# Performance work log

Hardware: AMD Instinct MI355X
Metric: run time of the kernel (lower is better)

The kernel has to match this reference:

```python
import jax, jax.numpy as jnp
import numpy as np

B, S_IN, S_CTX = 2, 4096, 512
INPUT_DIM = CTX_DIM = DIM = 1024
NUM_HEADS = 16
HEAD_DIM = DIM // NUM_HEADS
BASE = 10000.0


def rms_norm(x, scale, eps=1e-6):
    xf = x.astype(jnp.float32)
    rrms = jax.lax.rsqrt(jnp.mean(xf * xf, axis=-1, keepdims=True) + eps)
    return (xf * rrms).astype(x.dtype) * scale


def apply_rope(x, pos):
    # x: [B, N, H, D]; rotate-half RoPE over full head_dim
    d = x.shape[-1]
    inv_freq = 1.0 / (BASE ** (jnp.arange(0, d, 2, dtype=jnp.float32) / d))  # [d/2]
    ang = pos.astype(jnp.float32)[:, None] * inv_freq[None, :]  # [N, d/2]
    cos = jnp.cos(ang)[None, :, None, :]
    sin = jnp.sin(ang)[None, :, None, :]
    x1, x2 = x[..., : d // 2], x[..., d // 2 :]
    return jnp.concatenate([x1 * cos - x2 * sin, x2 * cos + x1 * sin], axis=-1).astype(x.dtype)


def setup_inputs() -> dict:
    key = jax.random.key(0)
    ks = jax.random.split(key, 8)
    std = 0.02
    return {
        "input": jax.random.normal(ks[0], (B, S_IN, INPUT_DIM), jnp.float32),
        "context": jax.random.normal(ks[1], (B, S_CTX, CTX_DIM), jnp.float32),
        "W_qkv_in": jax.random.normal(ks[2], (3 * DIM, INPUT_DIM), jnp.float32) * std,
        "b_qkv_in": jnp.zeros((3 * DIM,), jnp.float32),
        "W_qkv_ctx": jax.random.normal(ks[3], (3 * DIM, CTX_DIM), jnp.float32) * std,
        "b_qkv_ctx": jnp.zeros((3 * DIM,), jnp.float32),
        "q_scale_in": jnp.ones((DIM,), jnp.float32),
        "k_scale_in": jnp.ones((DIM,), jnp.float32),
        "q_scale_ctx": jnp.ones((DIM,), jnp.float32),
        "k_scale_ctx": jnp.ones((DIM,), jnp.float32),
        "W_out_in": jax.random.normal(ks[4], (INPUT_DIM, DIM), jnp.float32) * std,
        "b_out_in": jnp.zeros((INPUT_DIM,), jnp.float32),
        "W_out_ctx": jax.random.normal(ks[5], (CTX_DIM, DIM), jnp.float32) * std,
        "b_out_ctx": jnp.zeros((CTX_DIM,), jnp.float32),
    }


def reference(input, context, W_qkv_in, b_qkv_in, W_qkv_ctx, b_qkv_ctx,
              q_scale_in, k_scale_in, q_scale_ctx, k_scale_ctx,
              W_out_in, b_out_in, W_out_ctx, b_out_ctx):
    # dual-stream QKV projections
    qkv_i = input @ W_qkv_in.T + b_qkv_in        # [B, S_in, 3*DIM]
    qkv_c = context @ W_qkv_ctx.T + b_qkv_ctx    # [B, S_ctx, 3*DIM]
    qi, ki, vi = jnp.split(qkv_i, 3, axis=-1)
    qc, kc, vc = jnp.split(qkv_c, 3, axis=-1)
    # QK-RMSNorm over full dim (as in QKNorm(dim))
    qi, ki = rms_norm(qi, q_scale_in), rms_norm(ki, k_scale_in)
    qc, kc = rms_norm(qc, q_scale_ctx), rms_norm(kc, k_scale_ctx)
    # concat context first, then input
    q = jnp.concatenate([qc, qi], axis=1)  # [B, N, DIM]
    k = jnp.concatenate([kc, ki], axis=1)
    v = jnp.concatenate([vc, vi], axis=1)
    N = q.shape[1]
    pos = jnp.arange(N)
    # RoPE applied per head
    q = apply_rope(q.reshape(B, N, NUM_HEADS, HEAD_DIM), pos).reshape(B, N, DIM)
    k = apply_rope(k.reshape(B, N, NUM_HEADS, HEAD_DIM), pos).reshape(B, N, DIM)
    # single-head attention over full dim (faithful to source: heads flattened before q@k^T)
    scale = HEAD_DIM ** -0.5
    attn = jax.nn.softmax(jnp.einsum('bnd,bmd->bnm', q, k) * scale, axis=-1)
    out = jnp.einsum('bnm,bmd->bnd', attn, v)  # [B, N, DIM]
    s_ctx = context.shape[1]
    input_output = out[:, s_ctx:, :] @ W_out_in.T + b_out_in
    context_output = out[:, :s_ctx, :] @ W_out_ctx.T + b_out_ctx
    return (input_output, context_output)
```

## Files before the change

kernel.cpp:

```cpp
#include <hip/hip_runtime.h>
#include <stdint.h>

typedef unsigned short u16;
typedef __bf16 bf16x8 __attribute__((ext_vector_type(8)));
typedef float f32x4 __attribute__((ext_vector_type(4)));

typedef const __attribute__((address_space(1))) uint32_t* gu32p;
typedef __attribute__((address_space(3))) uint32_t* lu32p;
#define GLOAD_LDS16(g, l) \
  __builtin_amdgcn_global_load_lds((gu32p)(const void*)(g), (lu32p)(void*)(l), 16, 0, 0)

static __device__ __forceinline__ u16 f2bf(float f) {
  uint32_t u = __builtin_bit_cast(uint32_t, f);
  return (u16)((u + 0x7FFFu + ((u >> 16) & 1u)) >> 16);
}
static __device__ __forceinline__ float bf2f(u16 h) {
  uint32_t u = ((uint32_t)h) << 16;
  return __builtin_bit_cast(float, u);
}

__global__ __launch_bounds__(256) void k_conv_all(
    const float* __restrict__ s0, u16* __restrict__ d0,
    const float* __restrict__ s1, u16* __restrict__ d1,
    const float* __restrict__ s2, u16* __restrict__ d2,
    const float* __restrict__ s3, u16* __restrict__ d3,
    const float* __restrict__ s4, u16* __restrict__ d4,
    const float* __restrict__ s5, u16* __restrict__ d5) {
  int b = blockIdx.x;
  const float* src; u16* dst; long off;
  if (b < 8192)       { src = s0; dst = d0; off = (long)b * 1024; }
  else if (b < 9216)  { src = s1; dst = d1; off = (long)(b - 8192) * 1024; }
  else if (b < 12288) { src = s2; dst = d2; off = (long)(b - 9216) * 1024; }
  else if (b < 15360) { src = s3; dst = d3; off = (long)(b - 12288) * 1024; }
  else if (b < 16384) { src = s4; dst = d4; off = (long)(b - 15360) * 1024; }
  else                { src = s5; dst = d5; off = (long)(b - 16384) * 1024; }
  long i = off + threadIdx.x * 4;
  const float4 v = *(const float4*)&src[i];
  ushort4 o;
  o.x = f2bf(v.x); o.y = f2bf(v.y); o.z = f2bf(v.z); o.w = f2bf(v.w);
  *(ushort4*)&dst[i] = o;
}

__device__ __forceinline__ void gemm_m97(const u16* __restrict__ A, const u16* __restrict__ Bt,
                                         int lda, int ldb, long row0, long col0,
                                         int kbeg, int kend, u16* smem, f32x4 acc[4][4]) {
  const int tid = threadIdx.x;
  const int l = tid & 63;
  const int w = tid >> 6;
  const int wm = w >> 1, wn = w & 1;
  const int lr = l & 15, kg = l >> 4;
  const int rs = (kg ^ ((lr >> 1) & 3)) * 8;
  const int r_l = tid >> 2;
  const int ssrc = ((tid & 3) ^ ((r_l >> 1) & 3)) * 8;
  const u16* gA = &A[(row0 + r_l) * (long)lda + ssrc];
  const u16* gB = &Bt[(col0 + r_l) * (long)ldb + ssrc];
  const int wofs = w * 512;

  for (int k0 = kbeg; k0 < kend; k0 += 32) {
    GLOAD_LDS16(gA + k0, smem + wofs);
    GLOAD_LDS16(gA + 64 * (long)lda + k0, smem + 2048 + wofs);
    GLOAD_LDS16(gB + k0, smem + 4096 + wofs);
    GLOAD_LDS16(gB + 64 * (long)ldb + k0, smem + 6144 + wofs);
    __syncthreads();
    bf16x8 af[4], bv[4];
#pragma unroll
    for (int i = 0; i < 4; ++i) {
      af[i] = *(const bf16x8*)&smem[(wm * 64 + i * 16 + lr) * 32 + rs];
      bv[i] = *(const bf16x8*)&smem[4096 + (wn * 64 + i * 16 + lr) * 32 + rs];
    }
#pragma unroll
    for (int mf = 0; mf < 4; ++mf)
#pragma unroll
      for (int nf = 0; nf < 4; ++nf)
        acc[mf][nf] = __builtin_amdgcn_mfma_f32_16x16x32_bf16(af[mf], bv[nf], acc[mf][nf], 0, 0, 0);
    __syncthreads();
  }
}

#define EPI_VARS                                   \
  const int l = threadIdx.x & 63;                  \
  const int w = threadIdx.x >> 6;                  \
  const int wm = w >> 1, wn = w & 1;               \
  const int mrow = (l >> 4) * 4, ncol = l & 15;

__global__ __launch_bounds__(256) void k_gemm_qkv(
    const u16* __restrict__ XIN, const u16* __restrict__ XCTX,
    const u16* __restrict__ WQI, const u16* __restrict__ WQC,
    const float* __restrict__ bqi, const float* __restrict__ bqc,
    u16* __restrict__ qb, u16* __restrict__ kb, u16* __restrict__ vt) {
  __shared__ u16 smem[8192];
  f32x4 acc[4][4] = {};
  const bool isCtx = blockIdx.x >= 64;
  const u16* X = isCtx ? XCTX : XIN;
  const u16* W = isCtx ? WQC : WQI;
  const float* bias = isCtx ? bqc : bqi;
  const int seg_start = isCtx ? 0 : 512;
  long row0 = (long)(isCtx ? blockIdx.x - 64 : blockIdx.x) * 128;
  long col0 = (long)blockIdx.y * 128;
  gemm_m97(X, W, 1024, 1024, row0, col0, 0, 1024, smem, acc);
  EPI_VARS
#pragma unroll
  for (int mf = 0; mf < 4; ++mf)
#pragma unroll
    for (int nf = 0; nf < 4; ++nf)
#pragma unroll
      for (int r = 0; r < 4; ++r) {
        int m = (int)row0 + wm * 64 + mf * 16 + mrow + r;
        int n = (int)col0 + wn * 64 + nf * 16 + ncol;
        float v = acc[mf][nf][r] + bias[n];
        int b, s;
        if (isCtx) { b = m >> 9; s = m & 511; } else { b = m >> 12; s = m & 4095; }
        long grow = (long)b * 4608 + seg_start + s;
        if (n < 1024)      qb[grow * 1024 + n] = f2bf(v);
        else if (n < 2048) kb[grow * 1024 + (n - 1024)] = f2bf(v);
        else               vt[((long)b * 1024 + (n - 2048)) * 4608 + seg_start + s] = f2bf(v);
      }
}

__global__ __launch_bounds__(256) void k_normrope(u16* __restrict__ qb, u16* __restrict__ kb,
                                                  const float* __restrict__ qsi, const float* __restrict__ ksi,
                                                  const float* __restrict__ qsc, const float* __restrict__ ksc) {
  __shared__ float sm[4];
  const int row = blockIdx.x;
  const int which = blockIdx.y;
  const int n = row % 4608;
  u16* buf = which ? kb : qb;
  const float* scale = which ? (n < 512 ? ksc : ksi) : (n < 512 ? qsc : qsi);
  u16* rp = buf + (long)row * 1024;
  const int t = threadIdx.x;
  const int h = t >> 4;
  const int jj = (t & 15) * 2;
  const int e1 = h * 64 + jj;
  const int e2 = e1 + 32;
  uint32_t u1 = *(const uint32_t*)&rp[e1];
  uint32_t u2 = *(const uint32_t*)&rp[e2];
  float x1a = bf2f((u16)u1), x1b = bf2f((u16)(u1 >> 16));
  float x2a = bf2f((u16)u2), x2b = bf2f((u16)(u2 >> 16));
  float ss = x1a * x1a + x1b * x1b + x2a * x2a + x2b * x2b;
#pragma unroll
  for (int o = 32; o; o >>= 1) ss += __shfl_xor(ss, o, 64);
  if ((t & 63) == 0) sm[t >> 6] = ss;
  __syncthreads();
  ss = sm[0] + sm[1] + sm[2] + sm[3];
  const float rr = rsqrtf(ss * (1.0f / 1024.0f) + 1e-6f);
  float s1a = scale[e1], s1b = scale[e1 + 1], s2a = scale[e2], s2b = scale[e2 + 1];
  x1a *= rr * s1a; x1b *= rr * s1b; x2a *= rr * s2a; x2b *= rr * s2b;
  const float c = -13.287712379549449f / 32.0f;
  float fa = exp2f((float)jj * c), fb = exp2f((float)(jj + 1) * c);
  float sna, csa, snb, csb;
  sincosf((float)n * fa, &sna, &csa);
  sincosf((float)n * fb, &snb, &csb);
  u16 o1a = f2bf(x1a * csa - x2a * sna), o1b = f2bf(x1b * csb - x2b * snb);
  u16 o2a = f2bf(x2a * csa + x1a * sna), o2b = f2bf(x2b * csb + x1b * snb);
  *(uint32_t*)&rp[e1] = (uint32_t)o1a | ((uint32_t)o1b << 16);
  *(uint32_t*)&rp[e2] = (uint32_t)o2a | ((uint32_t)o2b << 16);
}

__global__ __launch_bounds__(256) void k_gemm_s(const u16* __restrict__ Q, const u16* __restrict__ Kb,
                                                float* __restrict__ S) {
  __shared__ u16 smem[8192];
  f32x4 acc[4][4] = {};
  long row0 = (long)blockIdx.x * 128;
  long col0 = (long)blockIdx.y * 128;
  gemm_m97(Q, Kb, 1024, 1024, row0, col0, 0, 1024, smem, acc);
  EPI_VARS
#pragma unroll
  for (int mf = 0; mf < 4; ++mf)
#pragma unroll
    for (int nf = 0; nf < 4; ++nf)
#pragma unroll
      for (int r = 0; r < 4; ++r) {
        long m = row0 + wm * 64 + mf * 16 + mrow + r;
        long n = col0 + wn * 64 + nf * 16 + ncol;
        S[m * 4608 + n] = acc[mf][nf][r] * 0.125f;
      }
}

__global__ __launch_bounds__(256) void k_softmax(const float* __restrict__ S, u16* __restrict__ P) {
  __shared__ float sm[4];
  const long row = blockIdx.x;
  const float* sr = S + row * 4608;
  const int t = threadIdx.x;
  float v[18];
  float mx = -3.4e38f;
#pragma unroll
  for (int i = 0; i < 18; ++i) { v[i] = sr[i * 256 + t]; mx = fmaxf(mx, v[i]); }
#pragma unroll
  for (int o = 32; o; o >>= 1) mx = fmaxf(mx, __shfl_xor(mx, o, 64));
  if ((t & 63) == 0) sm[t >> 6] = mx;
  __syncthreads();
  mx = fmaxf(fmaxf(sm[0], sm[1]), fmaxf(sm[2], sm[3]));
  __syncthreads();
  float sum = 0.f;
#pragma unroll
  for (int i = 0; i < 18; ++i) { v[i] = __expf(v[i] - mx); sum += v[i]; }
#pragma unroll
  for (int o = 32; o; o >>= 1) sum += __shfl_xor(sum, o, 64);
  if ((t & 63) == 0) sm[t >> 6] = sum;
  __syncthreads();
  sum = sm[0] + sm[1] + sm[2] + sm[3];
  const float inv = 1.0f / sum;
  u16* pr = P + row * 4608;
#pragma unroll
  for (int i = 0; i < 18; ++i) pr[i * 256 + t] = f2bf(v[i] * inv);
}

__global__ __launch_bounds__(256) void k_gemm_o(const u16* __restrict__ P, const u16* __restrict__ VT,
                                                float* __restrict__ OP) {
  __shared__ u16 smem[8192];
  f32x4 acc[4][4] = {};
  long row0 = (long)blockIdx.x * 128;
  long col0 = (long)blockIdx.y * 128;
  const int kc = blockIdx.z;
  gemm_m97(P, VT, 4608, 4608, row0, col0, kc * 2304, (kc + 1) * 2304, smem, acc);
  float* op = OP + (long)kc * 4608 * 1024;
  EPI_VARS
#pragma unroll
  for (int mf = 0; mf < 4; ++mf)
#pragma unroll
    for (int nf = 0; nf < 4; ++nf)
#pragma unroll
      for (int r = 0; r < 4; ++r) {
        long m = row0 + wm * 64 + mf * 16 + mrow + r;
        long n = col0 + wn * 64 + nf * 16 + ncol;
        op[m * 1024 + n] = acc[mf][nf][r];
      }
}

__global__ __launch_bounds__(256) void k_reduce2(const float* __restrict__ OP, u16* __restrict__ AO) {
  const long st = 4608L * 1024;
  long i = ((long)blockIdx.x * 256 + threadIdx.x) * 4;
  float4 a = *(const float4*)&OP[i];
  float4 b = *(const float4*)&OP[i + st];
  ushort4 o;
  o.x = f2bf(a.x + b.x);
  o.y = f2bf(a.y + b.y);
  o.z = f2bf(a.z + b.z);
  o.w = f2bf(a.w + b.w);
  *(ushort4*)&AO[i] = o;
}

__global__ __launch_bounds__(256) void k_gemm_out2(const u16* __restrict__ AO,
                                                   const u16* __restrict__ WOI, const u16* __restrict__ WOC,
                                                   const float* __restrict__ boi, const float* __restrict__ boc,
                                                   float* __restrict__ out) {
  __shared__ u16 smem[8192];
  f32x4 acc[4][4] = {};
  long row0 = (long)blockIdx.x * 128;
  long col0 = (long)blockIdx.y * 128;
  int b = (int)(row0 / 4608);
  int s0 = (int)(row0 % 4608);
  const bool ctx = s0 < 512;
  const u16* W = ctx ? WOC : WOI;
  const float* bias = ctx ? boc : boi;
  float* ob = ctx ? out + 8388608 + ((long)b * 512 + s0) * 1024
                  : out + ((long)b * 4096 + (s0 - 512)) * 1024;
  gemm_m97(AO, W, 1024, 1024, row0, col0, 0, 1024, smem, acc);
  EPI_VARS
#pragma unroll
  for (int mf = 0; mf < 4; ++mf)
#pragma unroll
    for (int nf = 0; nf < 4; ++nf)
#pragma unroll
      for (int r = 0; r < 4; ++r) {
        long m = wm * 64 + mf * 16 + mrow + r;
        long n = col0 + wn * 64 + nf * 16 + ncol;
        ob[m * 1024 + n] = acc[mf][nf][r] + bias[n];
      }
}

extern "C" void kernel_launch(void* const* d_in, const int* in_sizes, int n_in,
                              void* d_out, int out_size, void* d_ws, size_t ws_size,
                              hipStream_t stream) {
  const float* input   = (const float*)d_in[0];
  const float* context = (const float*)d_in[1];
  const float* Wqi     = (const float*)d_in[2];
  const float* bqi     = (const float*)d_in[3];
  const float* Wqc     = (const float*)d_in[4];
  const float* bqc     = (const float*)d_in[5];
  const float* qsi     = (const float*)d_in[6];
  const float* ksi     = (const float*)d_in[7];
  const float* qsc     = (const float*)d_in[8];
  const float* ksc     = (const float*)d_in[9];
  const float* Woi     = (const float*)d_in[10];
  const float* boi     = (const float*)d_in[11];
  const float* Woc     = (const float*)d_in[12];
  const float* boc     = (const float*)d_in[13];
  float* out = (float*)d_out;

  uint8_t* ws = (uint8_t*)d_ws;
  u16* XIN  = (u16*)(ws + 0);
  u16* XCTX = (u16*)(ws + 16777216);
  u16* WQI  = (u16*)(ws + 18874368);
  u16* WQC  = (u16*)(ws + 25165824);
  u16* WOI  = (u16*)(ws + 31457280);
  u16* WOC  = (u16*)(ws + 33554432);
  u16* QB   = (u16*)(ws + 35651584);
  u16* KB   = (u16*)(ws + 54525952);
  u16* VT   = (u16*)(ws + 73400320);
  u16* AO   = (u16*)(ws + 92274688);
  float* S32 = (float*)(ws + 111149056);
  u16* PB   = (u16*)(ws + 196083712);

  k_conv_all<<<dim3(17408), 256, 0, stream>>>(input, XIN, context, XCTX, Wqi, WQI,
                                              Wqc, WQC, Woi, WOI, Woc, WOC);

  k_gemm_qkv<<<dim3(72, 24), 256, 0, stream>>>(XIN, XCTX, WQI, WQC, bqi, bqc, QB, KB, VT);

  k_normrope<<<dim3(9216, 2), 256, 0, stream>>>(QB, KB, qsi, ksi, qsc, ksc);

  for (int b = 0; b < 2; ++b) {
    const u16* Qb  = QB + (long)b * 4608 * 1024;
    const u16* Kbp = KB + (long)b * 4608 * 1024;
    const u16* VTb = VT + (long)b * 1024 * 4608;
    u16* AOb = AO + (long)b * 4608 * 1024;
    k_gemm_s<<<dim3(36, 36), 256, 0, stream>>>(Qb, Kbp, S32);
    k_softmax<<<dim3(4608), 256, 0, stream>>>(S32, PB);
    k_gemm_o<<<dim3(36, 8, 2), 256, 0, stream>>>(PB, VTb, (float*)S32);
    k_reduce2<<<dim3(4608), 256, 0, stream>>>((const float*)S32, AOb);
  }

  k_gemm_out2<<<dim3(72, 8), 256, 0, stream>>>(AO, WOI, WOC, boi, boc, out);
}
```

Before: 524.3 us.

## Replace GEMM core with 256x256 double-buffered pipelined 8-wave tile

Swaps the 128x128 single-buffered GEMM core for a 256x256 tile run by 512 threads. The new core uses 64-wide K steps, double-buffered LDS, staged global-to-LDS prefetch interleaved with MFMA quads, and s_setprio to raise priority around the MFMA bursts. All four GEMM kernels move to it, and the PV GEMM's split-K goes from 2 to 4 with a matching 4-way reduce. The aim is more operand reuse per LDS load and overlap of loads with compute. The trade-off is fewer blocks (some grids fall below the CU count), 128KB of LDS per block, and more partial-sum traffic.

```diff
diff --git a/kernel.cpp b/kernel.cpp
--- a/kernel.cpp
+++ b/kernel.cpp
@@ -9,6 +9,7 @@
 typedef __attribute__((address_space(3))) uint32_t* lu32p;
 #define GLOAD_LDS16(g, l) \
   __builtin_amdgcn_global_load_lds((gu32p)(const void*)(g), (lu32p)(void*)(l), 16, 0, 0)
+#define MFMA16 __builtin_amdgcn_mfma_f32_16x16x32_bf16
 
 static __device__ __forceinline__ u16 f2bf(float f) {
   uint32_t u = __builtin_bit_cast(uint32_t, f);
@@ -41,71 +42,113 @@
   *(ushort4*)&dst[i] = o;
 }
 
-__device__ __forceinline__ void gemm_m97(const u16* __restrict__ A, const u16* __restrict__ Bt,
-                                         int lda, int ldb, long row0, long col0,
-                                         int kbeg, int kend, u16* smem, f32x4 acc[4][4]) {
+__device__ __forceinline__ void gemm8p(const u16* __restrict__ A, const u16* __restrict__ Bt,
+                                       int lda, int ldb, long row0, long col0,
+                                       int kbeg, int kend, u16* smem, f32x4 acc[8][4]) {
   const int tid = threadIdx.x;
   const int l = tid & 63;
-  const int w = tid >> 6;
-  const int wm = w >> 1, wn = w & 1;
+  const int wid = tid >> 6;
+  const int wm = wid >> 2, wn = wid & 3;
   const int lr = l & 15, kg = l >> 4;
-  const int rs = (kg ^ ((lr >> 1) & 3)) * 8;
-  const int r_l = tid >> 2;
-  const int ssrc = ((tid & 3) ^ ((r_l >> 1) & 3)) * 8;
-  const u16* gA = &A[(row0 + r_l) * (long)lda + ssrc];
-  const u16* gB = &Bt[(col0 + r_l) * (long)ldb + ssrc];
-  const int wofs = w * 512;
-
-  for (int k0 = kbeg; k0 < kend; k0 += 32) {
-    GLOAD_LDS16(gA + k0, smem + wofs);
-    GLOAD_LDS16(gA + 64 * (long)lda + k0, smem + 2048 + wofs);
-    GLOAD_LDS16(gB + k0, smem + 4096 + wofs);
-    GLOAD_LDS16(gB + 64 * (long)ldb + k0, smem + 6144 + wofs);
-    __syncthreads();
-    bf16x8 af[4], bv[4];
-#pragma unroll
-    for (int i = 0; i < 4; ++i) {
-      af[i] = *(const bf16x8*)&smem[(wm * 64 + i * 16 + lr) * 32 + rs];
-      bv[i] = *(const bf16x8*)&smem[4096 + (wn * 64 + i * 16 + lr) * 32 + rs];
-    }
-#pragma unroll
-    for (int mf = 0; mf < 4; ++mf)
-#pragma unroll
-      for (int nf = 0; nf < 4; ++nf)
-        acc[mf][nf] = __builtin_amdgcn_mfma_f32_16x16x32_bf16(af[mf], bv[nf], acc[mf][nf], 0, 0, 0);
-    __syncthreads();
+  const int rx = lr & 7;
+  const int r_l = tid >> 3;
+  const int ss8 = ((tid & 7) ^ (r_l & 7)) * 8;
+  const u16* gA = &A[(row0 + r_l) * (long)lda + kbeg + ss8];
+  const u16* gB = &Bt[(col0 + r_l) * (long)ldb + kbeg + ss8];
+  const int wofs = wid * 512;
+  const int NK = (kend - kbeg) >> 6;
+
+#define STG_B0(s) if ((s) < NK) { const long kk = (long)(s) * 64; \
+    u16* bb = smem + ((s) & 1) * 32768 + 16384 + wofs; \
+    GLOAD_LDS16(gB + kk, bb); GLOAD_LDS16(gB + 64 * (long)ldb + kk, bb + 4096); }
+#define STG_B1(s) if ((s) < NK) { const long kk = (long)(s) * 64; \
+    u16* bb = smem + ((s) & 1) * 32768 + 16384 + 8192 + wofs; \
+    GLOAD_LDS16(gB + 128 * (long)ldb + kk, bb); GLOAD_LDS16(gB + 192 * (long)ldb + kk, bb + 4096); }
+#define STG_AL(s) if ((s) < NK) { const long kk = (long)(s) * 64; \
+    u16* bb = smem + ((s) & 1) * 32768 + wofs; \
+    GLOAD_LDS16(gA + kk, bb); GLOAD_LDS16(gA + 128 * (long)lda + kk, bb + 8192); }
+#define STG_AH(s) if ((s) < NK) { const long kk = (long)(s) * 64; \
+    u16* bb = smem + ((s) & 1) * 32768 + 4096 + wofs; \
+    GLOAD_LDS16(gA + 64 * (long)lda + kk, bb); GLOAD_LDS16(gA + 192 * (long)lda + kk, bb + 8192); }
+
+#define LDA_(db, mf, ks) (*(const bf16x8*)&smem[(db) + (wm * 128 + (mf) * 16 + lr) * 64 + (((ks) * 4 + kg) ^ rx) * 8])
+#define LDB_(db, nf, ks) (*(const bf16x8*)&smem[(db) + 16384 + (wn * 64 + (nf) * 16 + lr) * 64 + (((ks) * 4 + kg) ^ rx) * 8])
+
+#define BAR_MID() do { __builtin_amdgcn_s_barrier(); \
+    asm volatile("s_waitcnt lgkmcnt(0)" ::: "memory"); \
+    __builtin_amdgcn_sched_barrier(0); } while (0)
+#define QUAD(mf0) do { \
+    __builtin_amdgcn_s_setprio(1); \
+    _Pragma("unroll") \
+    for (int nf = 0; nf < 4; ++nf) { \
+      acc[(mf0)][nf]     = MFMA16(a00, bv0[nf], acc[(mf0)][nf], 0, 0, 0); \
+      acc[(mf0) + 1][nf] = MFMA16(a10, bv0[nf], acc[(mf0) + 1][nf], 0, 0, 0); \
+      acc[(mf0)][nf]     = MFMA16(a01, bv1[nf], acc[(mf0)][nf], 0, 0, 0); \
+      acc[(mf0) + 1][nf] = MFMA16(a11, bv1[nf], acc[(mf0) + 1][nf], 0, 0, 0); } \
+    __builtin_amdgcn_s_setprio(0); \
+    __builtin_amdgcn_s_barrier(); } while (0)
+
+  STG_B0(0); STG_B1(0); STG_AL(0); STG_AH(0);
+  STG_B0(1); STG_B1(1); STG_AL(1);
+  asm volatile("s_waitcnt vmcnt(6)" ::: "memory");
+  __builtin_amdgcn_s_barrier();
+  __builtin_amdgcn_sched_barrier(0);
+
+  for (int k = 0; k < NK; ++k) {
+    const int db = (k & 1) * 32768;
+    bf16x8 bv0[4], bv1[4], a00, a01, a10, a11;
+#pragma unroll
+    for (int nf = 0; nf < 4; ++nf) { bv0[nf] = LDB_(db, nf, 0); bv1[nf] = LDB_(db, nf, 1); }
+    a00 = LDA_(db, 0, 0); a01 = LDA_(db, 0, 1); a10 = LDA_(db, 1, 0); a11 = LDA_(db, 1, 1);
+    STG_AH(k + 1);
+    BAR_MID(); QUAD(0);
+    a00 = LDA_(db, 2, 0); a01 = LDA_(db, 2, 1); a10 = LDA_(db, 3, 0); a11 = LDA_(db, 3, 1);
+    STG_B0(k + 2);
+    BAR_MID(); QUAD(2);
+    a00 = LDA_(db, 4, 0); a01 = LDA_(db, 4, 1); a10 = LDA_(db, 5, 0); a11 = LDA_(db, 5, 1);
+    STG_B1(k + 2);
+    BAR_MID(); QUAD(4);
+    a00 = LDA_(db, 6, 0); a01 = LDA_(db, 6, 1); a10 = LDA_(db, 7, 0); a11 = LDA_(db, 7, 1);
+    STG_AL(k + 2);
+    if (k + 2 < NK) asm volatile("s_waitcnt vmcnt(6)" ::: "memory");
+    else            asm volatile("s_waitcnt vmcnt(0)" ::: "memory");
+    BAR_MID(); QUAD(6);
   }
-}
-
-#define EPI_VARS                                   \
+#undef STG_B0
+#undef STG_B1
+#undef STG_AL
+#undef STG_AH
+}
+
+#define EPI8                                       \
   const int l = threadIdx.x & 63;                  \
-  const int w = threadIdx.x >> 6;                  \
-  const int wm = w >> 1, wn = w & 1;               \
+  const int wid = threadIdx.x >> 6;                \
+  const int wm = wid >> 2, wn = wid & 3;           \
   const int mrow = (l >> 4) * 4, ncol = l & 15;
 
-__global__ __launch_bounds__(256) void k_gemm_qkv(
+__global__ __launch_bounds__(512, 2) void k_gemm_qkv(
     const u16* __restrict__ XIN, const u16* __restrict__ XCTX,
     const u16* __restrict__ WQI, const u16* __restrict__ WQC,
     const float* __restrict__ bqi, const float* __restrict__ bqc,
     u16* __restrict__ qb, u16* __restrict__ kb, u16* __restrict__ vt) {
-  __shared__ u16 smem[8192];
-  f32x4 acc[4][4] = {};
-  const bool isCtx = blockIdx.x >= 64;
+  __shared__ u16 smem[65536];
+  f32x4 acc[8][4] = {};
+  const bool isCtx = blockIdx.x >= 32;
   const u16* X = isCtx ? XCTX : XIN;
   const u16* W = isCtx ? WQC : WQI;
   const float* bias = isCtx ? bqc : bqi;
   const int seg_start = isCtx ? 0 : 512;
-  long row0 = (long)(isCtx ? blockIdx.x - 64 : blockIdx.x) * 128;
-  long col0 = (long)blockIdx.y * 128;
-  gemm_m97(X, W, 1024, 1024, row0, col0, 0, 1024, smem, acc);
-  EPI_VARS
-#pragma unroll
-  for (int mf = 0; mf < 4; ++mf)
+  long row0 = (long)(isCtx ? blockIdx.x - 32 : blockIdx.x) * 256;
+  long col0 = (long)blockIdx.y * 256;
+  gemm8p(X, W, 1024, 1024, row0, col0, 0, 1024, smem, acc);
+  EPI8
+#pragma unroll
+  for (int mf = 0; mf < 8; ++mf)
 #pragma unroll
     for (int nf = 0; nf < 4; ++nf)
 #pragma unroll
       for (int r = 0; r < 4; ++r) {
-        int m = (int)row0 + wm * 64 + mf * 16 + mrow + r;
+        int m = (int)row0 + wm * 128 + mf * 16 + mrow + r;
         int n = (int)col0 + wn * 64 + nf * 16 + ncol;
         float v = acc[mf][nf][r] + bias[n];
         int b, s;
@@ -156,21 +199,21 @@
   *(uint32_t*)&rp[e2] = (uint32_t)o2a | ((uint32_t)o2b << 16);
 }
 
-__global__ __launch_bounds__(256) void k_gemm_s(const u16* __restrict__ Q, const u16* __restrict__ Kb,
-                                                float* __restrict__ S) {
-  __shared__ u16 smem[8192];
-  f32x4 acc[4][4] = {};
-  long row0 = (long)blockIdx.x * 128;
-  long col0 = (long)blockIdx.y * 128;
-  gemm_m97(Q, Kb, 1024, 1024, row0, col0, 0, 1024, smem, acc);
-  EPI_VARS
-#pragma unroll
-  for (int mf = 0; mf < 4; ++mf)
+__global__ __launch_bounds__(512, 2) void k_gemm_s(const u16* __restrict__ Q, const u16* __restrict__ Kb,
+                                                   float* __restrict__ S) {
+  __shared__ u16 smem[65536];
+  f32x4 acc[8][4] = {};
+  long row0 = (long)blockIdx.x * 256;
+  long col0 = (long)blockIdx.y * 256;
+  gemm8p(Q, Kb, 1024, 1024, row0, col0, 0, 1024, smem, acc);
+  EPI8
+#pragma unroll
+  for (int mf = 0; mf < 8; ++mf)
 #pragma unroll
     for (int nf = 0; nf < 4; ++nf)
 #pragma unroll
       for (int r = 0; r < 4; ++r) {
-        long m = row0 + wm * 64 + mf * 16 + mrow + r;
+        long m = row0 + wm * 128 + mf * 16 + mrow + r;
         long n = col0 + wn * 64 + nf * 16 + ncol;
         S[m * 4608 + n] = acc[mf][nf][r] * 0.125f;
       }
@@ -205,49 +248,51 @@
   for (int i = 0; i < 18; ++i) pr[i * 256 + t] = f2bf(v[i] * inv);
 }
 
-__global__ __launch_bounds__(256) void k_gemm_o(const u16* __restrict__ P, const u16* __restrict__ VT,
-                                                float* __restrict__ OP) {
-  __shared__ u16 smem[8192];
-  f32x4 acc[4][4] = {};
-  long row0 = (long)blockIdx.x * 128;
-  long col0 = (long)blockIdx.y * 128;
+__global__ __launch_bounds__(512, 2) void k_gemm_o(const u16* __restrict__ P, const u16* __restrict__ VT,
+                                                   float* __restrict__ OP) {
+  __shared__ u16 smem[65536];
+  f32x4 acc[8][4] = {};
+  long row0 = (long)blockIdx.x * 256;
+  long col0 = (long)blockIdx.y * 256;
   const int kc = blockIdx.z;
-  gemm_m97(P, VT, 4608, 4608, row0, col0, kc * 2304, (kc + 1) * 2304, smem, acc);
+  gemm8p(P, VT, 4608, 4608, row0, col0, kc * 1152, (kc + 1) * 1152, smem, acc);
   float* op = OP + (long)kc * 4608 * 1024;
-  EPI_VARS
-#pragma unroll
-  for (int mf = 0; mf < 4; ++mf)
+  EPI8
+#pragma unroll
+  for (int mf = 0; mf < 8; ++mf)
 #pragma unroll
     for (int nf = 0; nf < 4; ++nf)
 #pragma unroll
       for (int r = 0; r < 4; ++r) {
-        long m = row0 + wm * 64 + mf * 16 + mrow + r;
+        long m = row0 + wm * 128 + mf * 16 + mrow + r;
         long n = col0 + wn * 64 + nf * 16 + ncol;
         op[m * 1024 + n] = acc[mf][nf][r];
       }
 }
 
-__global__ __launch_bounds__(256) void k_reduce2(const float* __restrict__ OP, u16* __restrict__ AO) {
+__global__ __launch_bounds__(256) void k_reduce4(const float* __restrict__ OP, u16* __restrict__ AO) {
   const long st = 4608L * 1024;
   long i = ((long)blockIdx.x * 256 + threadIdx.x) * 4;
   float4 a = *(const float4*)&OP[i];
   float4 b = *(const float4*)&OP[i + st];
+  float4 c = *(const float4*)&OP[i + 2 * st];
+  float4 d = *(const float4*)&OP[i + 3 * st];
   ushort4 o;
-  o.x = f2bf(a.x + b.x);
-  o.y = f2bf(a.y + b.y);
-  o.z = f2bf(a.z + b.z);
-  o.w = f2bf(a.w + b.w);
+  o.x = f2bf(a.x + b.x + c.x + d.x);
+  o.y = f2bf(a.y + b.y + c.y + d.y);
+  o.z = f2bf(a.z + b.z + c.z + d.z);
+  o.w = f2bf(a.w + b.w + c.w + d.w);
   *(ushort4*)&AO[i] = o;
 }
 
-__global__ __launch_bounds__(256) void k_gemm_out2(const u16* __restrict__ AO,
-                                                   const u16* __restrict__ WOI, const u16* __restrict__ WOC,
-                                                   const float* __restrict__ boi, const float* __restrict__ boc,
-                                                   float* __restrict__ out) {
-  __shared__ u16 smem[8192];
-  f32x4 acc[4][4] = {};
-  long row0 = (long)blockIdx.x * 128;
-  long col0 = (long)blockIdx.y * 128;
+__global__ __launch_bounds__(512, 2) void k_gemm_out2(const u16* __restrict__ AO,
+                                                      const u16* __restrict__ WOI, const u16* __restrict__ WOC,
+                                                      const float* __restrict__ boi, const float* __restrict__ boc,
+                                                      float* __restrict__ out) {
+  __shared__ u16 smem[65536];
+  f32x4 acc[8][4] = {};
+  long row0 = (long)blockIdx.x * 256;
+  long col0 = (long)blockIdx.y * 256;
   int b = (int)(row0 / 4608);
   int s0 = (int)(row0 % 4608);
   const bool ctx = s0 < 512;
@@ -255,15 +300,15 @@
   const float* bias = ctx ? boc : boi;
   float* ob = ctx ? out + 8388608 + ((long)b * 512 + s0) * 1024
                   : out + ((long)b * 4096 + (s0 - 512)) * 1024;
-  gemm_m97(AO, W, 1024, 1024, row0, col0, 0, 1024, smem, acc);
-  EPI_VARS
-#pragma unroll
-  for (int mf = 0; mf < 4; ++mf)
+  gemm8p(AO, W, 1024, 1024, row0, col0, 0, 1024, smem, acc);
+  EPI8
+#pragma unroll
+  for (int mf = 0; mf < 8; ++mf)
 #pragma unroll
     for (int nf = 0; nf < 4; ++nf)
 #pragma unroll
       for (int r = 0; r < 4; ++r) {
-        long m = wm * 64 + mf * 16 + mrow + r;
+        long m = wm * 128 + mf * 16 + mrow + r;
         long n = col0 + wn * 64 + nf * 16 + ncol;
         ob[m * 1024 + n] = acc[mf][nf][r] + bias[n];
       }
@@ -305,7 +350,7 @@
   k_conv_all<<<dim3(17408), 256, 0, stream>>>(input, XIN, context, XCTX, Wqi, WQI,
                                               Wqc, WQC, Woi, WOI, Woc, WOC);
 
-  k_gemm_qkv<<<dim3(72, 24), 256, 0, stream>>>(XIN, XCTX, WQI, WQC, bqi, bqc, QB, KB, VT);
+  k_gemm_qkv<<<dim3(36, 12), 512, 0, stream>>>(XIN, XCTX, WQI, WQC, bqi, bqc, QB, KB, VT);
 
   k_normrope<<<dim3(9216, 2), 256, 0, stream>>>(QB, KB, qsi, ksi, qsc, ksc);
 
@@ -314,11 +359,11 @@
     const u16* Kbp = KB + (long)b * 4608 * 1024;
     const u16* VTb = VT + (long)b * 1024 * 4608;
     u16* AOb = AO + (long)b * 4608 * 1024;
-    k_gemm_s<<<dim3(36, 36), 256, 0, stream>>>(Qb, Kbp, S32);
+    k_gemm_s<<<dim3(18, 18), 512, 0, stream>>>(Qb, Kbp, S32);
     k_softmax<<<dim3(4608), 256, 0, stream>>>(S32, PB);
-    k_gemm_o<<<dim3(36, 8, 2), 256, 0, stream>>>(PB, VTb, (float*)S32);
-    k_reduce2<<<dim3(4608), 256, 0, stream>>>((const float*)S32, AOb);
+    k_gemm_o<<<dim3(18, 4, 4), 512, 0, stream>>>(PB, VTb, (float*)S32);
+    k_reduce4<<<dim3(4608), 256, 0, stream>>>((const float*)S32, AOb);
   }
 
-  k_gemm_out2<<<dim3(72, 8), 256, 0, stream>>>(AO, WOI, WOC, boi, boc, out);
-}
+  k_gemm_out2<<<dim3(36, 4), 512, 0, stream>>>(AO, WOI, WOC, boi, boc, out);
+}
```

Measured after the change: 508.5 us. -3.0%, faster.
